# Performance work log

Measured on AMD Instinct MI355X. Metric: run time of the kernel, lower is better.

The kernel has to match this reference:

```python
import jax, jax.numpy as jnp
import numpy as np
import math

SEGMENT_LENGTHS = [2048, 4096, 8192]
DILATION_RATES = [1, 2, 4]


def setup_inputs() -> dict:
    key = jax.random.key(0)
    kq, kk, kv = jax.random.split(key, 3)
    b, n, h, d = 2, 8192, 32, 128
    q = jax.random.normal(kq, (b, n, h, d), dtype=jnp.float32)
    k = jax.random.normal(kk, (b, n, h, d), dtype=jnp.float32)
    v = jax.random.normal(kv, (b, n, h, d), dtype=jnp.float32)
    return {"q": q, "k": k, "v": v}


def _dilated_attention(q, k, v):
    # Faithful translation of _compute_dilated_attention.
    # NOTE: torch.matmul on (b, S, h, d) with transpose(-2, -1) contracts over
    # head_dim d and yields (b, S, h, h) scores: heads attend to heads at a
    # single (possibly dilated) key position. We reproduce that exactly.
    b, n, h, d = q.shape
    scale = 1.0 / math.sqrt(d)
    out = jnp.zeros_like(q)
    for seg_len, dil in zip(SEGMENT_LENGTHS, DILATION_RATES):
        if seg_len > n:
            continue
        n_seg = n // seg_len
        cov = n_seg * seg_len
        # (b, n_seg, seg_len, h, d)
        qs = q[:, :cov].reshape(b, n_seg, seg_len, h, d)
        if dil == 1:
            ks = k[:, :cov].reshape(b, n_seg, seg_len, h, d)
            vs = v[:, :cov].reshape(b, n_seg, seg_len, h, d)
        else:
            # idx[g, i] = g*seg_len + i*dil, clamped to n-1 (matches the loop)
            idx = (jnp.arange(n_seg)[:, None] * seg_len
                   + jnp.arange(seg_len)[None, :] * dil)
            idx = jnp.minimum(idx, n - 1)  # (n_seg, seg_len)
            ks = k[:, idx]  # (b, n_seg, seg_len, h, d)
            vs = v[:, idx]
        scores = jnp.einsum('bgsid,bgsjd->bgsij', qs, ks) * scale  # (b,g,s,h,h)
        attn = jax.nn.softmax(scores, axis=-1)
        res = jnp.einsum('bgsij,bgsjd->bgsid', attn, vs)
        # later configs overwrite earlier ones, as in the torch loop
        out = out.at[:, :cov].set(res.reshape(b, cov, h, d))
    return out


def reference(q, k, v):
    # world_size == 1 -> hierarchy level 1 -> _local_forward with all heads
    # local, which is just _compute_dilated_attention.
    return _dilated_attention(q, k, v)
```

## Files before the change

### kernel.cpp

```cpp
#include <hip/hip_runtime.h>
#include <hip/hip_bf16.h>

typedef __attribute__((ext_vector_type(4))) float f32x4;
typedef __attribute__((ext_vector_type(8))) __bf16 bf16x8;

#define NCTX 8192
#define DH 128
#define ROWE 4096
#define SC2 0.12751705766482797f
#define KSTR 136
#define PSTR 40
#define OSTR 132
#define BUFS (32*KSTR)

__device__ __forceinline__ unsigned f2bf(float x) {
  union { float f; unsigned u; } un; un.f = x;
  return (un.u + 0x7FFFu + ((un.u >> 16) & 1u)) >> 16;
}
__device__ __forceinline__ unsigned pk2(float a, float b) {
  float2 t; t.x = a; t.y = b;
  union { __hip_bfloat162 h; unsigned u; } un;
  un.h = __float22bfloat162_rn(t);
  return un.u;
}

__device__ __forceinline__ void stage_row(const float* __restrict__ src,
                                          unsigned short* dst, int lane) {
  const int jb = lane >> 5, d = 4 * (lane & 31);
#pragma unroll
  for (int half = 0; half < 2; ++half) {
    f32x4 x[8];
#pragma unroll
    for (int ch = 0; ch < 8; ++ch)
      x[ch] = *reinterpret_cast<const f32x4*>(src + 4*lane + 256*(half*8 + ch));
#pragma unroll
    for (int ch = 0; ch < 8; ++ch) {
      const int j = jb + 2*(half*8 + ch);
      uint2 wv;
      wv.x = pk2(x[ch][0], x[ch][1]);
      wv.y = pk2(x[ch][2], x[ch][3]);
      *reinterpret_cast<uint2*>(&dst[j*KSTR + d]) = wv;
    }
  }
}

__global__ __launch_bounds__(256, 3) void hda(
    const float* __restrict__ q, const float* __restrict__ kg,
    const float* __restrict__ v, float* __restrict__ out)
{
  extern __shared__ __align__(16) unsigned short lds[];

  const int tid  = threadIdx.x;
  const int w    = tid >> 6;
  const int lane = tid & 63;
  const int c = lane & 15;
  const int g = lane >> 4;

  const int pos = blockIdx.x * 4 + w;
  const int b = pos >> 13;
  const int s = pos & (NCTX - 1);
  const int s0 = (blockIdx.x * 4) & (NCTX - 1);
  const bool shared_kv = (s0 >= 2048);

  const float* qb_ = q  + (size_t)b * NCTX * ROWE;
  const float* kb_ = kg + (size_t)b * NCTX * ROWE;
  const float* vb_ = v  + (size_t)b * NCTX * ROWE;
  float*       op  = out + ((size_t)b * NCTX + s) * ROWE;

  unsigned short* sb = lds + w * BUFS;
  const unsigned short* kbuf = shared_kv ? (lds + 4*BUFS) : sb;
  const unsigned short* vbuf = shared_kv ? (lds + 5*BUFS) : sb;

  if (shared_kv) {
    const float* kr8 = kb_ + (size_t)(NCTX - 1) * ROWE;
    const float* vr8 = vb_ + (size_t)(NCTX - 1) * ROWE;
    const int d = 4 * (tid & 31), jb = tid >> 5;
#pragma unroll
    for (int ch = 0; ch < 4; ++ch) {
      const int fo = 4*tid + 1024*ch;
      const int j  = jb + 8*ch;
      f32x4 xk = *reinterpret_cast<const f32x4*>(kr8 + fo);
      f32x4 xv = *reinterpret_cast<const f32x4*>(vr8 + fo);
      uint2 wk, wv2;
      wk.x  = pk2(xk[0], xk[1]); wk.y  = pk2(xk[2], xk[3]);
      wv2.x = pk2(xv[0], xv[1]); wv2.y = pk2(xv[2], xv[3]);
      *reinterpret_cast<uint2*>(&lds[4*BUFS + j*KSTR + d]) = wk;
      *reinterpret_cast<uint2*>(&lds[5*BUFS + j*KSTR + d]) = wv2;
    }
    __syncthreads();
  }

  stage_row(qb_ + (size_t)s * ROWE, sb, lane);
  bf16x8 qa[2][4];
#pragma unroll
  for (int t = 0; t < 2; ++t)
#pragma unroll
    for (int ks = 0; ks < 4; ++ks)
      qa[t][ks] = *reinterpret_cast<const bf16x8*>(&sb[(t*16 + c)*KSTR + ks*32 + g*8]);

  if (!shared_kv)
    stage_row(kb_ + (size_t)(4*s) * ROWE, sb, lane);
  bf16x8 kf[2][4];
#pragma unroll
  for (int t = 0; t < 2; ++t)
#pragma unroll
    for (int ks = 0; ks < 4; ++ks)
      kf[t][ks] = *reinterpret_cast<const bf16x8*>(&kbuf[(t*16 + c)*KSTR + ks*32 + g*8]);

  if (!shared_kv)
    stage_row(vb_ + (size_t)(4*s) * ROWE, sb, lane);

  f32x4 S[2][2];
#pragma unroll
  for (int it = 0; it < 2; ++it)
#pragma unroll
    for (int jt = 0; jt < 2; ++jt) {
      f32x4 acc = (f32x4)0.0f;
#pragma unroll
      for (int ks = 0; ks < 4; ++ks)
        acc = __builtin_amdgcn_mfma_f32_16x16x32_bf16(qa[it][ks], kf[jt][ks], acc, 0, 0, 0);
      S[it][jt] = acc;
    }

  float p[2][2][4], inv[2][4];
#pragma unroll
  for (int it = 0; it < 2; ++it) {
    float ls[4] = {0.f, 0.f, 0.f, 0.f};
#pragma unroll
    for (int jt = 0; jt < 2; ++jt)
#pragma unroll
      for (int rr = 0; rr < 4; ++rr) {
        float e = exp2f(S[it][jt][rr] * SC2);
        p[it][jt][rr] = e;
        ls[rr] += e;
      }
#pragma unroll
    for (int m = 1; m <= 8; m <<= 1)
#pragma unroll
      for (int rr = 0; rr < 4; ++rr)
        ls[rr] += __shfl_xor(ls[rr], m);
#pragma unroll
    for (int rr = 0; rr < 4; ++rr) inv[it][rr] = 1.0f / ls[rr];
  }

  bf16x8 va[8];
#pragma unroll
  for (int dt = 0; dt < 8; ++dt) {
    unsigned t0 = vbuf[(g*8 + 0)*KSTR + dt*16 + c];
    unsigned t1 = vbuf[(g*8 + 1)*KSTR + dt*16 + c];
    unsigned t2 = vbuf[(g*8 + 2)*KSTR + dt*16 + c];
    unsigned t3 = vbuf[(g*8 + 3)*KSTR + dt*16 + c];
    unsigned t4 = vbuf[(g*8 + 4)*KSTR + dt*16 + c];
    unsigned t5 = vbuf[(g*8 + 5)*KSTR + dt*16 + c];
    unsigned t6 = vbuf[(g*8 + 6)*KSTR + dt*16 + c];
    unsigned t7 = vbuf[(g*8 + 7)*KSTR + dt*16 + c];
    union { unsigned u[4]; bf16x8 f; } un;
    un.u[0] = t0 | (t1 << 16); un.u[1] = t2 | (t3 << 16);
    un.u[2] = t4 | (t5 << 16); un.u[3] = t6 | (t7 << 16);
    va[dt] = un.f;
  }

#pragma unroll
  for (int it = 0; it < 2; ++it)
#pragma unroll
    for (int jt = 0; jt < 2; ++jt)
#pragma unroll
      for (int rr = 0; rr < 4; ++rr)
        sb[(it*16 + g*4 + rr)*PSTR + jt*16 + c] =
            (unsigned short)f2bf(p[it][jt][rr] * inv[it][rr]);

  bf16x8 pa[2];
  pa[0] = *reinterpret_cast<const bf16x8*>(&sb[c*PSTR + g*8]);
  pa[1] = *reinterpret_cast<const bf16x8*>(&sb[(16 + c)*PSTR + g*8]);

  float* ob = reinterpret_cast<float*>(sb);
#pragma unroll
  for (int it = 0; it < 2; ++it) {
    f32x4 o[8];
#pragma unroll
    for (int dt = 0; dt < 8; ++dt)
      o[dt] = __builtin_amdgcn_mfma_f32_16x16x32_bf16(va[dt], pa[it], (f32x4)0.0f, 0, 0, 0);
#pragma unroll
    for (int dt = 0; dt < 8; ++dt)
      *reinterpret_cast<f32x4*>(&ob[c*OSTR + dt*16 + g*4]) = o[dt];
#pragma unroll
    for (int ch = 0; ch < 8; ++ch) {
      const int flat = 4*lane + 256*ch;
      const int row = flat >> 7, col = flat & 127;
      f32x4 y = *reinterpret_cast<const f32x4*>(&ob[row*OSTR + col]);
      *reinterpret_cast<f32x4*>(op + it*2048 + flat) = y;
    }
  }
}

extern "C" void kernel_launch(void* const* d_in, const int* in_sizes, int n_in,
                              void* d_out, int out_size, void* d_ws, size_t ws_size,
                              hipStream_t stream) {
  const float* q = (const float*)d_in[0];
  const float* k = (const float*)d_in[1];
  const float* v = (const float*)d_in[2];
  float* o = (float*)d_out;
  hda<<<dim3(4096, 1, 1), dim3(256, 1, 1), 6 * BUFS * 2, stream>>>(q, k, v, o);
}
```

Before: 132.7 us.

## Overlap V row loads with QK MFMA and softmax; use nontemporal Q loads and output stores

The V-row staging is split into two halves. Each half's global loads are issued before the QK MFMAs or the softmax, and sched barriers keep the compiler from moving them, so memory latency overlaps with compute. Q loads and output stores now use nontemporal hints, meant to keep streamed data out of cache and leave room for reused K/V rows. This raises register pressure from holding eight f32x4 values live, which could hurt occupancy under launch_bounds(256,3).

New measurement: 113.5 us. 1.17x faster.

```diff
diff --git a/kernel.cpp b/kernel.cpp
--- a/kernel.cpp
+++ b/kernel.cpp
@@ -24,6 +24,7 @@
   return un.u;
 }
 
+template<bool NT>
 __device__ __forceinline__ void stage_row(const float* __restrict__ src,
                                           unsigned short* dst, int lane) {
   const int jb = lane >> 5, d = 4 * (lane & 31);
@@ -31,8 +32,10 @@
   for (int half = 0; half < 2; ++half) {
     f32x4 x[8];
 #pragma unroll
-    for (int ch = 0; ch < 8; ++ch)
-      x[ch] = *reinterpret_cast<const f32x4*>(src + 4*lane + 256*(half*8 + ch));
+    for (int ch = 0; ch < 8; ++ch) {
+      const f32x4* p = reinterpret_cast<const f32x4*>(src + 4*lane + 256*(half*8 + ch));
+      x[ch] = NT ? __builtin_nontemporal_load(p) : *p;
+    }
 #pragma unroll
     for (int ch = 0; ch < 8; ++ch) {
       const int j = jb + 2*(half*8 + ch);
@@ -55,6 +58,7 @@
   const int lane = tid & 63;
   const int c = lane & 15;
   const int g = lane >> 4;
+  const int jb = lane >> 5, dcol = 4 * (lane & 31);
 
   const int pos = blockIdx.x * 4 + w;
   const int b = pos >> 13;
@@ -74,11 +78,11 @@
   if (shared_kv) {
     const float* kr8 = kb_ + (size_t)(NCTX - 1) * ROWE;
     const float* vr8 = vb_ + (size_t)(NCTX - 1) * ROWE;
-    const int d = 4 * (tid & 31), jb = tid >> 5;
+    const int d = 4 * (tid & 31), jj = tid >> 5;
 #pragma unroll
     for (int ch = 0; ch < 4; ++ch) {
       const int fo = 4*tid + 1024*ch;
-      const int j  = jb + 8*ch;
+      const int j  = jj + 8*ch;
       f32x4 xk = *reinterpret_cast<const f32x4*>(kr8 + fo);
       f32x4 xv = *reinterpret_cast<const f32x4*>(vr8 + fo);
       uint2 wk, wv2;
@@ -90,7 +94,7 @@
     __syncthreads();
   }
 
-  stage_row(qb_ + (size_t)s * ROWE, sb, lane);
+  stage_row<true>(qb_ + (size_t)s * ROWE, sb, lane);
   bf16x8 qa[2][4];
 #pragma unroll
   for (int t = 0; t < 2; ++t)
@@ -98,8 +102,9 @@
     for (int ks = 0; ks < 4; ++ks)
       qa[t][ks] = *reinterpret_cast<const bf16x8*>(&sb[(t*16 + c)*KSTR + ks*32 + g*8]);
 
+  const float* vsrc = vb_ + (size_t)(4*s) * ROWE;
   if (!shared_kv)
-    stage_row(kb_ + (size_t)(4*s) * ROWE, sb, lane);
+    stage_row<false>(kb_ + (size_t)(4*s) * ROWE, sb, lane);
   bf16x8 kf[2][4];
 #pragma unroll
   for (int t = 0; t < 2; ++t)
@@ -107,8 +112,13 @@
     for (int ks = 0; ks < 4; ++ks)
       kf[t][ks] = *reinterpret_cast<const bf16x8*>(&kbuf[(t*16 + c)*KSTR + ks*32 + g*8]);
 
-  if (!shared_kv)
-    stage_row(vb_ + (size_t)(4*s) * ROWE, sb, lane);
+  f32x4 vx[8];
+  if (!shared_kv) {
+#pragma unroll
+    for (int ch = 0; ch < 8; ++ch)
+      vx[ch] = *reinterpret_cast<const f32x4*>(vsrc + 4*lane + 256*ch);
+    __builtin_amdgcn_sched_barrier(0);
+  }
 
   f32x4 S[2][2];
 #pragma unroll
@@ -121,6 +131,20 @@
         acc = __builtin_amdgcn_mfma_f32_16x16x32_bf16(qa[it][ks], kf[jt][ks], acc, 0, 0, 0);
       S[it][jt] = acc;
     }
+
+  if (!shared_kv) {
+#pragma unroll
+    for (int ch = 0; ch < 8; ++ch) {
+      uint2 wv;
+      wv.x = pk2(vx[ch][0], vx[ch][1]);
+      wv.y = pk2(vx[ch][2], vx[ch][3]);
+      *reinterpret_cast<uint2*>(&sb[(jb + 2*ch)*KSTR + dcol]) = wv;
+    }
+#pragma unroll
+    for (int ch = 0; ch < 8; ++ch)
+      vx[ch] = *reinterpret_cast<const f32x4*>(vsrc + 4*lane + 256*(8 + ch));
+    __builtin_amdgcn_sched_barrier(0);
+  }
 
   float p[2][2][4], inv[2][4];
 #pragma unroll
@@ -141,6 +165,16 @@
         ls[rr] += __shfl_xor(ls[rr], m);
 #pragma unroll
     for (int rr = 0; rr < 4; ++rr) inv[it][rr] = 1.0f / ls[rr];
+  }
+
+  if (!shared_kv) {
+#pragma unroll
+    for (int ch = 0; ch < 8; ++ch) {
+      uint2 wv;
+      wv.x = pk2(vx[ch][0], vx[ch][1]);
+      wv.y = pk2(vx[ch][2], vx[ch][3]);
+      *reinterpret_cast<uint2*>(&sb[(jb + 2*(8 + ch))*KSTR + dcol]) = wv;
+    }
   }
 
   bf16x8 va[8];
@@ -188,7 +222,7 @@
       const int flat = 4*lane + 256*ch;
       const int row = flat >> 7, col = flat & 127;
       f32x4 y = *reinterpret_cast<const f32x4*>(&ob[row*OSTR + col]);
-      *reinterpret_cast<f32x4*>(op + it*2048 + flat) = y;
+      __builtin_nontemporal_store(y, reinterpret_cast<f32x4*>(op + it*2048 + flat));
     }
   }
 }
```
